# Performance work log

Hardware: AMD Instinct MI355X
Metric: run time of the kernel (lower is better)

The kernel has to match this reference:

```python
import jax, jax.numpy as jnp
import numpy as np

B, S, D_H, D_L, K, K_H, W = 4, 4096, 1024, 256, 64, 4, 9


def setup_inputs() -> dict:
    key = jax.random.key(0)
    ks = jax.random.split(key, 6)
    return {
        "inputs": jax.random.normal(ks[0], (B, S, D_H), jnp.float32),
        "W1": jax.random.normal(ks[1], (D_H, D_L), jnp.float32) * 0.02,
        "b1": jnp.zeros((D_L,), jnp.float32),
        "RME": jax.random.normal(ks[2], (D_L, K), jnp.float32),
        "K2": jax.random.normal(ks[3], (K_H, D_L, D_L), jnp.float32) * 0.02,
        "b2": jnp.zeros((D_L,), jnp.float32),
        "Wu": jax.random.normal(ks[4], (D_L, D_H), jnp.float32) * 0.02,
        "bu": jnp.zeros((D_H,), jnp.float32),
        "gamma": jnp.ones((D_H,), jnp.float32),
        "beta": jnp.zeros((D_H,), jnp.float32),
    }


def _memory_reorg(act, RMVs, k_h):
    # act: [B,S,d_l], RMVs: [B,S,k]
    R = jnp.transpose(RMVs, (0, 2, 1))  # [B,k,S]
    h_vars = jnp.mean((R - jnp.mean(R, axis=-1, keepdims=True)) ** 2, axis=-1)  # [B,k]
    top = jnp.argsort(-h_vars, axis=-1)[:, :k_h]                   # [B,k_h]
    h_max = jnp.take_along_axis(R, top[:, :, None], axis=1)        # [B,k_h,S]
    perm = jnp.argsort(h_max, axis=-1)                             # [B,k_h,S] permutation indices
    g = jnp.take_along_axis(act[:, None], perm[..., None], axis=2) # [B,k_h,S,d_l]
    return jnp.transpose(g, (0, 2, 1, 3))                          # [B,S,k_h,d_l]


def reference(inputs, W1, b1, RME, K2, b2, Wu, bu, gamma, beta):
    # DOWN_PROJECTION_1
    q = jax.nn.relu(jnp.einsum('bsh,hd->bsd', inputs, W1) + b1)    # [B,S,d_l]
    # RANDOM_PROJECTION
    RMVs = jnp.einsum('bsd,dk->bsk', q, RME)                       # [B,S,k]
    # Memory reorganization (variance-based argsort permutations)
    qp = _memory_reorg(q, RMVs, K_H)                               # [B,S,k_h,d_l]
    # DOWN_PROJECTION_2
    q2 = jax.nn.relu(jnp.einsum('bskd,kde->bse', qp, K2) + b2)     # [B,S,d_l]
    # Sliding-window key construction (edge windows replicated)
    half = (W - 1) // 2
    widx = jnp.arange(S - W + 1)[:, None] + jnp.arange(W)[None, :]  # [S-W+1, W]
    win = q2[:, widx]                                               # [B,S-W+1,W,d_l]
    first = jnp.broadcast_to(q2[:, None, :W], (B, half, W, D_L))
    last = jnp.broadcast_to(q2[:, None, S - W:], (B, half, W, D_L))
    keyt = jnp.concatenate([first, win, last], axis=1)              # [B,S,W,d_l]
    # Windowed attention
    f = jnp.sqrt(jnp.float32(D_L))
    scores = jax.nn.softmax(jnp.einsum('bsd,bswd->bsw', q2, keyt) / f, axis=-1)  # [B,S,W]
    # UP_PROJECTION on keys -> values
    val = jax.nn.relu(jnp.einsum('bswd,dh->bswh', keyt, Wu) + bu)   # [B,S,W,d_h]
    out = jnp.einsum('bswh,bsw->bsh', val, scores)                  # [B,S,d_h]
    # LayerNorm (keras default epsilon=1e-3) on residual
    x = out + inputs
    mu = jnp.mean(x, axis=-1, keepdims=True)
    var = jnp.mean((x - mu) ** 2, axis=-1, keepdims=True)
    return gamma * (x - mu) * jax.lax.rsqrt(var + 1e-3) + beta
```

## Files before the change

kernel.cpp:

```cpp
#include <hip/hip_runtime.h>

#define B_  4
#define S_  4096
#define DH  1024
#define DL  256
#define KK  64
#define KH  4
#define WW  9

typedef unsigned short ushort_t;
typedef _Float16 f16;
typedef _Float16 f16x8 __attribute__((ext_vector_type(8)));
typedef float  f32x4  __attribute__((ext_vector_type(4)));

__device__ __forceinline__ void gld_lds16(const void* g, void* lds_uniform_base) {
    __builtin_amdgcn_global_load_lds(
        (const __attribute__((address_space(1))) unsigned int*)g,
        (__attribute__((address_space(3))) unsigned int*)lds_uniform_base,
        16, 0, 0);
}

__global__ __launch_bounds__(256)
void mfma_gemm2(const float* __restrict__ Af,
                const ushort_t* __restrict__ Bh, const ushort_t* __restrict__ Bl,
                const float* __restrict__ bias, float* __restrict__ C,
                ushort_t* __restrict__ Ch, int K, int N, int nbx)
{
    __shared__ __align__(16) ushort_t Abuf[64 * 64 * 2];
    __shared__ __align__(16) ushort_t Bsh[128 * 64];
    __shared__ __align__(16) ushort_t Bsl[128 * 64];

    const int tid = threadIdx.x;
    const int w = tid >> 6, l = tid & 63;
    const int wm = w >> 1, wn = w & 1;
    const int lr = l & 15, lk = l >> 4;
    const int cpx = gridDim.x >> 3;
    const int orig = (blockIdx.x & 7) * cpx + (blockIdx.x >> 3);
    const int m0 = (orig / nbx) * 64, n0 = (orig % nbx) * 128;

    f32x4 acc0[2][4] = {};
    f32x4 acc1[2][4] = {};

    for (int k0 = 0; k0 < K; k0 += 64) {
        {
            float* Asf = (float*)Abuf;
            #pragma unroll
            for (int it = 0; it < 4; ++it) {
                const int c = it * 256 + tid;
                const int r = c >> 4, cc = c & 15;
                const int cs = cc ^ ((r & 7) << 1);
                const float* src = Af + (size_t)(m0 + r) * K + k0 + cs * 4;
                gld_lds16(src, &Asf[(size_t)c * 4]);
            }
        }
        #pragma unroll
        for (int it = 0; it < 4; ++it) {
            const int c = it * 256 + tid;
            const int r = c >> 3, kp = c & 7;
            const int kl = kp ^ (r & 7);
            const size_t off = (size_t)(n0 + r) * K + k0 + kl * 8;
            gld_lds16(Bh + off, &Bsh[(size_t)c * 8]);
            gld_lds16(Bl + off, &Bsl[(size_t)c * 8]);
        }
        __syncthreads();

        #pragma unroll
        for (int ks = 0; ks < 2; ++ks) {
            f16x8 ah[2], al[2];
            #pragma unroll
            for (int mf = 0; mf < 2; ++mf) {
                const int row = wm * 32 + mf * 16 + lr;
                const int kb  = ks * 4 + lk;
                const float* Asf = (const float*)Abuf;
                const int fo = row * 64 + ((kb ^ (row & 7)) << 3);
                const f32x4 lo = *(const f32x4*)&Asf[fo];
                const f32x4 hi = *(const f32x4*)&Asf[fo + 4];
                const float xs[8] = {lo[0], lo[1], lo[2], lo[3],
                                     hi[0], hi[1], hi[2], hi[3]};
                #pragma unroll
                for (int e = 0; e < 8; ++e) {
                    const f16 h = (f16)xs[e];
                    const f16 lv = (f16)((xs[e] - (float)h) * 2048.0f);
                    ah[mf][e] = h;
                    al[mf][e] = lv;
                }
            }
            #pragma unroll
            for (int nf = 0; nf < 4; ++nf) {
                const int row = wn * 64 + nf * 16 + lr;
                const int kb  = ks * 4 + lk;
                const int o   = row * 64 + ((kb ^ (row & 7)) << 3);
                const f16x8 bh = *(const f16x8*)&Bsh[o];
                const f16x8 bl = *(const f16x8*)&Bsl[o];
                #pragma unroll
                for (int mf = 0; mf < 2; ++mf) {
                    acc0[mf][nf] = __builtin_amdgcn_mfma_f32_16x16x32_f16(
                        ah[mf], bh, acc0[mf][nf], 0, 0, 0);
                    acc1[mf][nf] = __builtin_amdgcn_mfma_f32_16x16x32_f16(
                        ah[mf], bl, acc1[mf][nf], 0, 0, 0);
                    acc1[mf][nf] = __builtin_amdgcn_mfma_f32_16x16x32_f16(
                        al[mf], bh, acc1[mf][nf], 0, 0, 0);
                }
            }
        }
        __syncthreads();
    }

    float bv[4];
    #pragma unroll
    for (int nf = 0; nf < 4; ++nf)
        bv[nf] = bias[n0 + wn * 64 + nf * 16 + lr];
    #pragma unroll
    for (int mf = 0; mf < 2; ++mf)
        #pragma unroll
        for (int nf = 0; nf < 4; ++nf)
            #pragma unroll
            for (int r = 0; r < 4; ++r) {
                const int m = m0 + wm * 32 + mf * 16 + lk * 4 + r;
                const int n = n0 + wn * 64 + nf * 16 + lr;
                float x = acc0[mf][nf][r] + acc1[mf][nf][r] * (1.0f / 2048.0f) + bv[nf];
                x = fmaxf(x, 0.f);
                C[(size_t)m * N + n] = x;
                const f16 h = (f16)x;
                Ch[(size_t)m * N + n] = __builtin_bit_cast(ushort_t, h);
            }
}

__global__ __launch_bounds__(256)
void gemm6_1l(const ushort_t* __restrict__ Ah, const ushort_t* __restrict__ Bh,
              const float* __restrict__ bias, ushort_t* __restrict__ Ch,
              const int* __restrict__ gidx, int K, int N, int nbx)
{
    __shared__ __align__(16) ushort_t Ash[64 * 64];
    __shared__ __align__(16) ushort_t Bsh[128 * 64];

    const int tid = threadIdx.x;
    const int w = tid >> 6, l = tid & 63;
    const int wm = w >> 1, wn = w & 1;
    const int lr = l & 15, lk = l >> 4;
    const int cpx = gridDim.x >> 3;
    const int orig = (blockIdx.x & 7) * cpx + (blockIdx.x >> 3);
    const int m0 = (orig / nbx) * 64, n0 = (orig % nbx) * 128;

    f32x4 acc0[2][4] = {};

    for (int k0 = 0; k0 < K; k0 += 64) {
        #pragma unroll
        for (int it = 0; it < 2; ++it) {
            const int c = it * 256 + tid;
            const int r = c >> 3, kp = c & 7;
            const int kl = kp ^ (r & 7);
            const int rg = gidx[(m0 + r) * KH + (k0 >> 8)];
            const size_t off = (size_t)rg * DL + (k0 & (DL - 1)) + kl * 8;
            gld_lds16(Ah + off, &Ash[(size_t)c * 8]);
        }
        #pragma unroll
        for (int it = 0; it < 4; ++it) {
            const int c = it * 256 + tid;
            const int r = c >> 3, kp = c & 7;
            const int kl = kp ^ (r & 7);
            const size_t off = (size_t)(n0 + r) * K + k0 + kl * 8;
            gld_lds16(Bh + off, &Bsh[(size_t)c * 8]);
        }
        __syncthreads();

        #pragma unroll
        for (int ks = 0; ks < 2; ++ks) {
            f16x8 ah[2];
            #pragma unroll
            for (int mf = 0; mf < 2; ++mf) {
                const int row = wm * 32 + mf * 16 + lr;
                const int kb  = ks * 4 + lk;
                ah[mf] = *(const f16x8*)&Ash[row * 64 + ((kb ^ (row & 7)) << 3)];
            }
            #pragma unroll
            for (int nf = 0; nf < 4; ++nf) {
                const int row = wn * 64 + nf * 16 + lr;
                const int kb  = ks * 4 + lk;
                const f16x8 bh = *(const f16x8*)&Bsh[row * 64 + ((kb ^ (row & 7)) << 3)];
                #pragma unroll
                for (int mf = 0; mf < 2; ++mf)
                    acc0[mf][nf] = __builtin_amdgcn_mfma_f32_16x16x32_f16(
                        ah[mf], bh, acc0[mf][nf], 0, 0, 0);
            }
        }
        __syncthreads();
    }

    float bv[4];
    #pragma unroll
    for (int nf = 0; nf < 4; ++nf)
        bv[nf] = bias[n0 + wn * 64 + nf * 16 + lr];
    #pragma unroll
    for (int mf = 0; mf < 2; ++mf)
        #pragma unroll
        for (int nf = 0; nf < 4; ++nf)
            #pragma unroll
            for (int r = 0; r < 4; ++r) {
                const int m = m0 + wm * 32 + mf * 16 + lk * 4 + r;
                const int n = n0 + wn * 64 + nf * 16 + lr;
                float x = acc0[mf][nf][r] + bv[nf];
                x = fmaxf(x, 0.f);
                const f16 h = (f16)x;
                Ch[(size_t)m * N + n] = __builtin_bit_cast(ushort_t, h);
            }
}

__global__ __launch_bounds__(512)
void mfma_gemm1l(const ushort_t* __restrict__ Ah, const ushort_t* __restrict__ Bh,
                 const float* __restrict__ bias, ushort_t* __restrict__ Ch,
                 int K, int N, int nbx)
{
    __shared__ __align__(16) ushort_t Ash[128 * 64];
    __shared__ __align__(16) ushort_t Bsh[128 * 64];

    const int tid = threadIdx.x;
    const int w = tid >> 6, l = tid & 63;
    const int wm = w >> 1, wn = w & 1;
    const int lr = l & 15, lk = l >> 4;
    const int cpx = gridDim.x >> 3;
    const int orig = (blockIdx.x & 7) * cpx + (blockIdx.x >> 3);
    const int m0 = (orig / nbx) * 128, n0 = (orig % nbx) * 128;

    f32x4 acc0[2][4] = {};

    for (int k0 = 0; k0 < K; k0 += 64) {
        #pragma unroll
        for (int it = 0; it < 2; ++it) {
            const int c = it * 512 + tid;
            const int r = c >> 3, kp = c & 7;
            const int kl = kp ^ (r & 7);
            const size_t offA = (size_t)(m0 + r) * K + k0 + kl * 8;
            const size_t offB = (size_t)(n0 + r) * K + k0 + kl * 8;
            gld_lds16(Ah + offA, &Ash[(size_t)c * 8]);
            gld_lds16(Bh + offB, &Bsh[(size_t)c * 8]);
        }
        __syncthreads();

        #pragma unroll
        for (int ks = 0; ks < 2; ++ks) {
            f16x8 ah[2];
            #pragma unroll
            for (int mf = 0; mf < 2; ++mf) {
                const int row = wm * 32 + mf * 16 + lr;
                const int kb  = ks * 4 + lk;
                ah[mf] = *(const f16x8*)&Ash[row * 64 + ((kb ^ (row & 7)) << 3)];
            }
            #pragma unroll
            for (int nf = 0; nf < 4; ++nf) {
                const int row = wn * 64 + nf * 16 + lr;
                const int kb  = ks * 4 + lk;
                const f16x8 bh = *(const f16x8*)&Bsh[row * 64 + ((kb ^ (row & 7)) << 3)];
                #pragma unroll
                for (int mf = 0; mf < 2; ++mf)
                    acc0[mf][nf] = __builtin_amdgcn_mfma_f32_16x16x32_f16(
                        ah[mf], bh, acc0[mf][nf], 0, 0, 0);
            }
        }
        __syncthreads();
    }

    float bv[4];
    #pragma unroll
    for (int nf = 0; nf < 4; ++nf)
        bv[nf] = bias[n0 + wn * 64 + nf * 16 + lr];
    #pragma unroll
    for (int mf = 0; mf < 2; ++mf)
        #pragma unroll
        for (int nf = 0; nf < 4; ++nf)
            #pragma unroll
            for (int r = 0; r < 4; ++r) {
                const int m = m0 + wm * 32 + mf * 16 + lk * 4 + r;
                const int n = n0 + wn * 64 + nf * 16 + lr;
                float x = acc0[mf][nf][r] + bv[nf];
                x = fmaxf(x, 0.f);
                const f16 hcv = (f16)x;
                Ch[(size_t)m * N + n] = __builtin_bit_cast(ushort_t, hcv);
            }
}

__global__ __launch_bounds__(256)
void tsplit2_kernel(const float* __restrict__ in, ushort_t* __restrict__ t0,
                    ushort_t* __restrict__ t1, int K, int N)
{
    __shared__ float tile[32][33];
    const int t = threadIdx.x;
    const int bk = blockIdx.x * 32, bn = blockIdx.y * 32;
    const int c = t & 31, rb = t >> 5;
    #pragma unroll
    for (int i = 0; i < 4; ++i) {
        const int r = rb + i * 8;
        tile[r][c] = in[(size_t)(bk + r) * N + bn + c];
    }
    __syncthreads();
    #pragma unroll
    for (int i = 0; i < 4; ++i) {
        const int rr = rb + i * 8;
        const float x = tile[c][rr];
        const f16 hv = (f16)x;
        const f16 lv = (f16)((x - (float)hv) * 2048.0f);
        const size_t o = (size_t)(bn + rr) * K + bk + c;
        t0[o] = __builtin_bit_cast(ushort_t, hv);
        t1[o] = __builtin_bit_cast(ushort_t, lv);
    }
}

__global__ __launch_bounds__(256)
void gemm_trans_kernel(const float* __restrict__ A, const float* __restrict__ Bm,
                       float* __restrict__ C, int M, int KA, int N)
{
    constexpr int BK = 16;
    __shared__ float Asb[BK][64 + 4];
    __shared__ float Bsb[BK][64 + 4];
    const int tid = threadIdx.x;
    const int tx = tid & 15, ty = tid >> 4;
    const int m0 = blockIdx.y * 64, n0 = blockIdx.x * 64;

    float acc[4][4] = {};
    const int lr = tid >> 2, lc = (tid & 3) << 2;
    const int kr = tid >> 4, nc = (tid & 15) << 2;

    for (int k0 = 0; k0 < KA; k0 += BK) {
        const float4 a4 = *reinterpret_cast<const float4*>(A + (size_t)(m0 + lr) * KA + k0 + lc);
        const float4 b4 = *reinterpret_cast<const float4*>(Bm + (size_t)(k0 + kr) * N + n0 + nc);
        Asb[lc + 0][lr] = a4.x; Asb[lc + 1][lr] = a4.y;
        Asb[lc + 2][lr] = a4.z; Asb[lc + 3][lr] = a4.w;
        *reinterpret_cast<float4*>(&Bsb[kr][nc]) = b4;
        __syncthreads();
        #pragma unroll
        for (int kk = 0; kk < BK; ++kk) {
            const float4 av = *reinterpret_cast<const float4*>(&Asb[kk][ty << 2]);
            const float4 bv = *reinterpret_cast<const float4*>(&Bsb[kk][tx << 2]);
            const float a[4] = {av.x, av.y, av.z, av.w};
            const float b[4] = {bv.x, bv.y, bv.z, bv.w};
            #pragma unroll
            for (int i = 0; i < 4; ++i)
                #pragma unroll
                for (int j = 0; j < 4; ++j)
                    acc[i][j] = fmaf(a[i], b[j], acc[i][j]);
        }
        __syncthreads();
    }
    #pragma unroll
    for (int i = 0; i < 4; ++i) {
        const int m = m0 + (ty << 2) + i;
        const int b = m >> 12, s = m & (S_ - 1);
        #pragma unroll
        for (int j = 0; j < 4; ++j) {
            const int n = n0 + (tx << 2) + j;
            C[(size_t)(b * N + n) * S_ + s] = acc[i][j];
        }
    }
}

__global__ __launch_bounds__(256)
void var_kernel(const float* __restrict__ rmvT, float* __restrict__ hvars)
{
    const int bk = blockIdx.x;
    const float* src = rmvT + (size_t)bk * S_;
    float s1 = 0.f, s2 = 0.f;
    for (int t = threadIdx.x; t < S_; t += 256) {
        const float v = src[t];
        s1 += v; s2 += v * v;
    }
    #pragma unroll
    for (int off = 32; off; off >>= 1) {
        s1 += __shfl_xor(s1, off);
        s2 += __shfl_xor(s2, off);
    }
    __shared__ float r1[4], r2[4];
    const int wave = threadIdx.x >> 6, lane = threadIdx.x & 63;
    if (lane == 0) { r1[wave] = s1; r2[wave] = s2; }
    __syncthreads();
    if (threadIdx.x == 0) {
        const float t1 = r1[0] + r1[1] + r1[2] + r1[3];
        const float t2 = r2[0] + r2[1] + r2[2] + r2[3];
        const float mu = t1 / (float)S_;
        hvars[bk] = t2 / (float)S_ - mu * mu;
    }
}

__global__ void topk_kernel(const float* __restrict__ hvars, int* __restrict__ topidx)
{
    const int b = threadIdx.x;
    if (b >= B_) return;
    float v[KK];
    for (int k = 0; k < KK; ++k) v[k] = hvars[b * KK + k];
    for (int i = 0; i < KH; ++i) {
        int best = 0; float bv = -3.4e38f;
        for (int k = 0; k < KK; ++k)
            if (v[k] > bv) { bv = v[k]; best = k; }
        topidx[b * KH + i] = best;
        v[best] = -3.4e38f;
    }
}

__global__ __launch_bounds__(256)
void rank_kernel(const float* __restrict__ rmvT, const int* __restrict__ topidx,
                 int* __restrict__ gidx)
{
    const int bi = blockIdx.x;
    const int b = bi >> 2, ih = bi & 3;
    const int k = topidx[b * KH + ih];
    const float* src = rmvT + (size_t)(b * KK + k) * S_;
    __shared__ __align__(16) unsigned long long keys[S_];
    __shared__ int partial[4][64];
    for (int t = threadIdx.x; t < S_; t += 256) {
        const unsigned bits = __builtin_bit_cast(unsigned, src[t]);
        const unsigned u = (bits & 0x80000000u) ? ~bits : (bits | 0x80000000u);
        keys[t] = ((unsigned long long)u << 12) | (unsigned)t;
    }
    __syncthreads();

    const int il = threadIdx.x & 63;
    const int chunk = threadIdx.x >> 6;
    const int i = blockIdx.y * 64 + il;
    const unsigned long long ki = keys[i];

    int cnt = 0;
    const int jbase = chunk << 10;
    #pragma unroll 8
    for (int jj = 0; jj < 1024; jj += 2) {
        const ulonglong2 k2 = *reinterpret_cast<const ulonglong2*>(&keys[jbase + jj]);
        cnt += (int)(k2.x < ki);
        cnt += (int)(k2.y < ki);
    }
    partial[chunk][il] = cnt;
    __syncthreads();
    if (threadIdx.x < 64) {
        const int rank = partial[0][threadIdx.x] + partial[1][threadIdx.x]
                       + partial[2][threadIdx.x] + partial[3][threadIdx.x];
        const int ii = blockIdx.y * 64 + threadIdx.x;
        gidx[((b << 12) + rank) * KH + ih] = (b << 12) + ii;
    }
}

__global__ __launch_bounds__(256)
void final_kernel(const ushort_t* __restrict__ vh, const ushort_t* __restrict__ q2h,
                  const float* __restrict__ inputs, const float* __restrict__ gamma,
                  const float* __restrict__ beta, float* __restrict__ out)
{
    const int bid = blockIdx.x;
    const int m0 = (((bid & 7) << 9) | (bid >> 3)) << 2;
    const int wave = threadIdx.x >> 6, lane = threadIdx.x & 63;
    const int m = m0 + wave;
    const int s = m & (S_ - 1), b = m >> 12;
    const int jb = (s < 4) ? 0 : (s >= S_ - 4 ? S_ - WW : s - 4);

    const ushort_t* vb = vh + (size_t)(b * S_ + jb) * DH;
    const float* inp = inputs + (size_t)m * DH;
    f16x8 varr[2][WW];
    float4 iv[2][2];
    #pragma unroll
    for (int c = 0; c < 2; ++c) {
        const int h = (c << 9) + (lane << 3);
        #pragma unroll
        for (int w = 0; w < WW; ++w)
            varr[c][w] = *reinterpret_cast<const f16x8*>(vb + (size_t)w * DH + h);
        iv[c][0] = *reinterpret_cast<const float4*>(inp + h);
        iv[c][1] = *reinterpret_cast<const float4*>(inp + h + 4);
    }

    const ushort4 qv4 = *reinterpret_cast<const ushort4*>(q2h + (size_t)m * DL + (lane << 2));
    const float qx = (float)__builtin_bit_cast(f16, qv4.x);
    const float qy = (float)__builtin_bit_cast(f16, qv4.y);
    const float qz = (float)__builtin_bit_cast(f16, qv4.z);
    const float qw = (float)__builtin_bit_cast(f16, qv4.w);
    const ushort_t* kbase = q2h + (size_t)(b * S_ + jb) * DL;
    float sc[WW];
    #pragma unroll
    for (int w = 0; w < WW; ++w) {
        const ushort4 kv4 = *reinterpret_cast<const ushort4*>(kbase + w * DL + (lane << 2));
        float d = qx * (float)__builtin_bit_cast(f16, kv4.x)
                + qy * (float)__builtin_bit_cast(f16, kv4.y)
                + qz * (float)__builtin_bit_cast(f16, kv4.z)
                + qw * (float)__builtin_bit_cast(f16, kv4.w);
        #pragma unroll
        for (int off = 32; off; off >>= 1) d += __shfl_xor(d, off);
        sc[w] = d * 0.0625f;
    }
    float mx = sc[0];
    #pragma unroll
    for (int w = 1; w < WW; ++w) mx = fmaxf(mx, sc[w]);
    float wgt[WW]; float sum = 0.f;
    #pragma unroll
    for (int w = 0; w < WW; ++w) { wgt[w] = __expf(sc[w] - mx); sum += wgt[w]; }
    const float inv = 1.f / sum;
    #pragma unroll
    for (int w = 0; w < WW; ++w) wgt[w] *= inv;

    float x[2][8];
    float s1 = 0.f, s2 = 0.f;
    #pragma unroll
    for (int c = 0; c < 2; ++c) {
        float acc[8] = {};
        #pragma unroll
        for (int w = 0; w < WW; ++w) {
            const f16x8 vv = varr[c][w];
            #pragma unroll
            for (int e = 0; e < 8; ++e)
                acc[e] = fmaf(wgt[w], (float)vv[e], acc[e]);
        }
        #pragma unroll
        for (int e = 0; e < 8; ++e) {
            const float ivv = (e < 4) ? (&iv[c][0].x)[e] : (&iv[c][1].x)[e - 4];
            acc[e] += ivv;
            x[c][e] = acc[e];
            s1 += acc[e];
            s2 += acc[e] * acc[e];
        }
    }

    #pragma unroll
    for (int off = 32; off; off >>= 1) {
        s1 += __shfl_xor(s1, off);
        s2 += __shfl_xor(s2, off);
    }
    const float mu = s1 / (float)DH;
    const float rs = rsqrtf(s2 / (float)DH - mu * mu + 0.001f);

    #pragma unroll
    for (int c = 0; c < 2; ++c) {
        const int h = (c << 9) + (lane << 3);
        #pragma unroll
        for (int half = 0; half < 2; ++half) {
            const float4 g  = *reinterpret_cast<const float4*>(gamma + h + half * 4);
            const float4 bt = *reinterpret_cast<const float4*>(beta + h + half * 4);
            float4 o;
            o.x = g.x * (x[c][half * 4 + 0] - mu) * rs + bt.x;
            o.y = g.y * (x[c][half * 4 + 1] - mu) * rs + bt.y;
            o.z = g.z * (x[c][half * 4 + 2] - mu) * rs + bt.z;
            o.w = g.w * (x[c][half * 4 + 3] - mu) * rs + bt.w;
            *reinterpret_cast<float4*>(out + (size_t)m * DH + h + half * 4) = o;
        }
    }
}

extern "C" void kernel_launch(void* const* d_in, const int* in_sizes, int n_in,
                              void* d_out, int out_size, void* d_ws, size_t ws_size,
                              hipStream_t stream)
{
    (void)in_sizes; (void)n_in; (void)out_size; (void)ws_size;
    const float* inputs = (const float*)d_in[0];
    const float* W1     = (const float*)d_in[1];
    const float* b1     = (const float*)d_in[2];
    const float* RME    = (const float*)d_in[3];
    const float* K2     = (const float*)d_in[4];
    const float* b2     = (const float*)d_in[5];
    const float* Wu     = (const float*)d_in[6];
    const float* bu     = (const float*)d_in[7];
    const float* gamma  = (const float*)d_in[8];
    const float* beta   = (const float*)d_in[9];
    float* out = (float*)d_out;

    char* ws = (char*)d_ws;
    const size_t MB = 1u << 20;
    ushort_t* vh  = (ushort_t*)(ws + 0 * MB);
    float*    q   = (float*)   (ws + 64 * MB);
    ushort_t* qh  = (ushort_t*)(ws + 80 * MB);
    ushort_t* q2h = (ushort_t*)(ws + 112 * MB);
    float*    rmvT= (float*)   (ws + 128 * MB);
    float*    hvars  = (float*)(ws + 132 * MB);
    int*      topidx = (int*)  (ws + 132 * MB + 4096);
    int*      gidx   = (int*)  (ws + 132 * MB + 8192);
    ushort_t* w1th = (ushort_t*)(ws + 133 * MB);
    ushort_t* w1tl = w1th + (DH * DL);
    ushort_t* k2th = w1tl + (DH * DL);
    ushort_t* k2tl = k2th + (KH * DL * DL);
    ushort_t* wuth = k2tl + (KH * DL * DL);
    ushort_t* wutl = wuth + (DL * DH);

    const int M = B_ * S_;

    tsplit2_kernel<<<dim3(DH / 32, DL / 32), dim3(256), 0, stream>>>(W1, w1th, w1tl, DH, DL);
    tsplit2_kernel<<<dim3(KH * DL / 32, DL / 32), dim3(256), 0, stream>>>((const float*)K2, k2th, k2tl, KH * DL, DL);
    tsplit2_kernel<<<dim3(DL / 32, DH / 32), dim3(256), 0, stream>>>(Wu, wuth, wutl, DL, DH);

    mfma_gemm2<<<dim3((DL / 128) * (M / 64)), dim3(256), 0, stream>>>(
        inputs, w1th, w1tl, b1, q, qh, DH, DL, DL / 128);
    gemm_trans_kernel<<<dim3(KK / 64, M / 64), dim3(256), 0, stream>>>(q, RME, rmvT, M, DL, KK);
    var_kernel<<<dim3(B_ * KK), dim3(256), 0, stream>>>(rmvT, hvars);
    topk_kernel<<<dim3(1), dim3(64), 0, stream>>>(hvars, topidx);
    rank_kernel<<<dim3(B_ * KH, S_ / 64), dim3(256), 0, stream>>>(rmvT, topidx, gidx);
    gemm6_1l<<<dim3((DL / 128) * (M / 64)), dim3(256), 0, stream>>>(
        qh, k2th, b2, q2h, gidx, KH * DL, DL, DL / 128);
    mfma_gemm1l<<<dim3((DH / 128) * (M / 128)), dim3(512), 0, stream>>>(
        q2h, wuth, bu, vh, DL, DH, DH / 128);
    final_kernel<<<dim3(M / 4), dim3(256), 0, stream>>>(vh, q2h, inputs, gamma, beta, out);
}
```

Before: 165.6 us.

## Refine LDS swizzle, coalesce transposed RMV stores, drop unused low-half weight splits

Extends the A-tile XOR swizzle in the first GEMM with an extra bit and swaps the lo/hi float4 read order on alternating row groups, aiming to cut LDS bank conflicts. The transposed store of the random projection output now goes through a shared-memory tile, so global writes along S are coalesced instead of strided. K2 and Wu are now converted only to a high fp16 half with a new single-output transpose kernel, which skips computing and writing low halves the later GEMMs apparently never read. The extra shared tile raises LDS use in gemm_trans_kernel.

```diff
diff --git a/kernel.cpp b/kernel.cpp
--- a/kernel.cpp
+++ b/kernel.cpp
@@ -48,7 +48,8 @@
             for (int it = 0; it < 4; ++it) {
                 const int c = it * 256 + tid;
                 const int r = c >> 4, cc = c & 15;
-                const int cs = cc ^ ((r & 7) << 1);
+                const int hsw = ((r & 7) << 1) | ((r >> 3) & 1);
+                const int cs = cc ^ hsw;
                 const float* src = Af + (size_t)(m0 + r) * K + k0 + cs * 4;
                 gld_lds16(src, &Asf[(size_t)c * 4]);
             }
@@ -72,9 +73,10 @@
                 const int row = wm * 32 + mf * 16 + lr;
                 const int kb  = ks * 4 + lk;
                 const float* Asf = (const float*)Abuf;
-                const int fo = row * 64 + ((kb ^ (row & 7)) << 3);
-                const f32x4 lo = *(const f32x4*)&Asf[fo];
-                const f32x4 hi = *(const f32x4*)&Asf[fo + 4];
+                const int base = row * 64 + ((kb ^ (row & 7)) << 3);
+                const int sw = ((row >> 3) & 1) << 2;
+                const f32x4 lo = *(const f32x4*)&Asf[base + sw];
+                const f32x4 hi = *(const f32x4*)&Asf[base + (4 - sw)];
                 const float xs[8] = {lo[0], lo[1], lo[2], lo[3],
                                      hi[0], hi[1], hi[2], hi[3]};
                 #pragma unroll
@@ -306,12 +308,35 @@
 }
 
 __global__ __launch_bounds__(256)
+void tsplit1_kernel(const float* __restrict__ in, ushort_t* __restrict__ t0,
+                    int K, int N)
+{
+    __shared__ float tile[32][33];
+    const int t = threadIdx.x;
+    const int bk = blockIdx.x * 32, bn = blockIdx.y * 32;
+    const int c = t & 31, rb = t >> 5;
+    #pragma unroll
+    for (int i = 0; i < 4; ++i) {
+        const int r = rb + i * 8;
+        tile[r][c] = in[(size_t)(bk + r) * N + bn + c];
+    }
+    __syncthreads();
+    #pragma unroll
+    for (int i = 0; i < 4; ++i) {
+        const int rr = rb + i * 8;
+        const f16 hv = (f16)tile[c][rr];
+        t0[(size_t)(bn + rr) * K + bk + c] = __builtin_bit_cast(ushort_t, hv);
+    }
+}
+
+__global__ __launch_bounds__(256)
 void gemm_trans_kernel(const float* __restrict__ A, const float* __restrict__ Bm,
                        float* __restrict__ C, int M, int KA, int N)
 {
     constexpr int BK = 16;
     __shared__ float Asb[BK][64 + 4];
     __shared__ float Bsb[BK][64 + 4];
+    __shared__ float tileT[64][65];
     const int tid = threadIdx.x;
     const int tx = tid & 15, ty = tid >> 4;
     const int m0 = blockIdx.y * 64, n0 = blockIdx.x * 64;
@@ -341,15 +366,21 @@
         }
         __syncthreads();
     }
-    #pragma unroll
-    for (int i = 0; i < 4; ++i) {
-        const int m = m0 + (ty << 2) + i;
-        const int b = m >> 12, s = m & (S_ - 1);
-        #pragma unroll
-        for (int j = 0; j < 4; ++j) {
-            const int n = n0 + (tx << 2) + j;
-            C[(size_t)(b * N + n) * S_ + s] = acc[i][j];
-        }
+
+    #pragma unroll
+    for (int i = 0; i < 4; ++i)
+        #pragma unroll
+        for (int j = 0; j < 4; ++j)
+            tileT[(tx << 2) + j][(ty << 2) + i] = acc[i][j];
+    __syncthreads();
+
+    const int b = m0 >> 12;
+    const int s0 = m0 & (S_ - 1);
+    #pragma unroll
+    for (int rr = 0; rr < 16; ++rr) {
+        const int idx = rr * 256 + tid;
+        const int kl = idx >> 6, sl = idx & 63;
+        C[(size_t)(b * N + n0 + kl) * S_ + s0 + sl] = tileT[kl][sl];
     }
 }
 
@@ -566,15 +597,13 @@
     ushort_t* w1th = (ushort_t*)(ws + 133 * MB);
     ushort_t* w1tl = w1th + (DH * DL);
     ushort_t* k2th = w1tl + (DH * DL);
-    ushort_t* k2tl = k2th + (KH * DL * DL);
-    ushort_t* wuth = k2tl + (KH * DL * DL);
-    ushort_t* wutl = wuth + (DL * DH);
+    ushort_t* wuth = k2th + (KH * DL * DL);
 
     const int M = B_ * S_;
 
     tsplit2_kernel<<<dim3(DH / 32, DL / 32), dim3(256), 0, stream>>>(W1, w1th, w1tl, DH, DL);
-    tsplit2_kernel<<<dim3(KH * DL / 32, DL / 32), dim3(256), 0, stream>>>((const float*)K2, k2th, k2tl, KH * DL, DL);
-    tsplit2_kernel<<<dim3(DL / 32, DH / 32), dim3(256), 0, stream>>>(Wu, wuth, wutl, DL, DH);
+    tsplit1_kernel<<<dim3(KH * DL / 32, DL / 32), dim3(256), 0, stream>>>((const float*)K2, k2th, KH * DL, DL);
+    tsplit1_kernel<<<dim3(DL / 32, DH / 32), dim3(256), 0, stream>>>(Wu, wuth, DL, DH);
 
     mfma_gemm2<<<dim3((DL / 128) * (M / 64)), dim3(256), 0, stream>>>(
         inputs, w1th, w1tl, b1, q, qh, DH, DL, DL / 128);
```

Result: no change. 166.5 us (+0.5%).
